# Performance work log

Measured on AMD Instinct MI355X. Metric: run time of the kernel, lower is better.

The kernel has to match this reference:

```python
import jax, jax.numpy as jnp
import numpy as np

N = 100000
E = 1600000
F_IN = 128
F_OUT = 200


def setup_inputs() -> dict:
    key = jax.random.key(0)
    ks = jax.random.split(key, 10)
    x = jax.random.normal(ks[0], (N, F_IN), dtype=jnp.float32)
    edge_index = jax.random.randint(ks[1], (2, E), 0, N, dtype=jnp.int64)
    edge_weight = jax.random.uniform(ks[2], (E,), dtype=jnp.float32)
    s = 1.0 / np.sqrt(F_IN)
    W1 = jax.random.uniform(ks[3], (1, F_IN, F_OUT), dtype=jnp.float32, minval=-s, maxval=s)
    b1 = jnp.zeros((F_OUT,), dtype=jnp.float32)
    W2 = jax.random.uniform(ks[4], (2, F_IN, F_OUT), dtype=jnp.float32, minval=-s, maxval=s)
    b2 = jnp.zeros((F_OUT,), dtype=jnp.float32)
    W3 = jax.random.uniform(ks[5], (3, F_IN, F_OUT), dtype=jnp.float32, minval=-s, maxval=s)
    b3 = jnp.zeros((F_OUT,), dtype=jnp.float32)
    return {"x": x, "edge_index": edge_index, "edge_weight": edge_weight,
            "W1": W1, "b1": b1, "W2": W2, "b2": b2, "W3": W3, "b3": b3}


def _cheb_norm(edge_index, edge_weight, n):
    # PyG ChebConv norm with lambda_max=2.0: scaled Laplacian L_hat = L - I
    # off-diagonal entries: -w_ij * d_i^{-1/2} * d_j^{-1/2}; diagonal: 0
    row, col = edge_index[0], edge_index[1]
    deg = jax.ops.segment_sum(edge_weight, row, num_segments=n)
    dis = jnp.where(deg > 0, jax.lax.rsqrt(jnp.where(deg > 0, deg, 1.0)), 0.0)
    return -edge_weight * dis[row] * dis[col]


def _propagate(h, row, col, norm, n):
    # h: [N, F] -> sum over incoming edges of norm_e * h[col_e]
    return jax.ops.segment_sum(norm[:, None] * h[col], row, num_segments=n)


def _chebconv(x, row, col, norm, W, b, n):
    K = W.shape[0]
    Tx_prev2 = x
    out = jnp.einsum('nf,fo->no', x, W[0])
    if K > 1:
        Tx_prev = _propagate(x, row, col, norm, n)
        out = out + jnp.einsum('nf,fo->no', Tx_prev, W[1])
        for k in range(2, K):
            Tx_k = 2.0 * _propagate(Tx_prev, row, col, norm, n) - Tx_prev2
            out = out + jnp.einsum('nf,fo->no', Tx_k, W[k])
            Tx_prev2, Tx_prev = Tx_prev, Tx_k
    return out + b


def reference(x, edge_index, edge_weight, W1, b1, W2, b2, W3, b3):
    n = x.shape[0]
    row, col = edge_index[0], edge_index[1]
    norm = _cheb_norm(edge_index, edge_weight, n)
    scale_1 = _chebconv(x, row, col, norm, W1, b1, n)
    scale_2 = _chebconv(x, row, col, norm, W2, b2, n)
    scale_3 = _chebconv(x, row, col, norm, W3, b3, n)
    return (scale_1, scale_2, scale_3)
```

## Files before the change

kernel.cpp:

```cpp
#include <hip/hip_runtime.h>
#include <hip/hip_bf16.h>
#include <stdint.h>

#define NN    100000
#define NROWP 100096
#define NE    1600000
#define FIN   128
#define FOUT  200
#define NBLK  391

typedef __attribute__((ext_vector_type(8))) short short8;
typedef __attribute__((ext_vector_type(8))) unsigned short ushort8;
typedef __attribute__((ext_vector_type(2))) float f32x2;
typedef __attribute__((ext_vector_type(4))) float f32x4;
typedef __attribute__((ext_vector_type(2))) unsigned int u32x2;
typedef __attribute__((ext_vector_type(4))) unsigned int uint32x4;

__device__ __forceinline__ short f2bf(float f) {
    __hip_bfloat16 h = __float2bfloat16(f);
    return *reinterpret_cast<short*>(&h);
}
__device__ __forceinline__ unsigned short f2bfu(float f) {
    __hip_bfloat16 h = __float2bfloat16(f);
    return *reinterpret_cast<unsigned short*>(&h);
}
__device__ __forceinline__ float bf2f(unsigned short u) {
    return __uint_as_float((unsigned)u << 16);
}
__device__ __forceinline__ int getidx(const void* ei, int isI32, long long i) {
    return isI32 ? ((const int*)ei)[i] : (int)((const long long*)ei)[i];
}

__global__ void detect_kernel(const long long* ei64, int* flag) {
    int t = blockIdx.x * blockDim.x + threadIdx.x;
    long long v = ei64[t];
    if (v < 0 || v >= NN) atomicOr(flag, 1);
}

__global__ void cnt8_kernel(const void* ei, const int* flag, int* cnt8) {
    int e = blockIdx.x * blockDim.x + threadIdx.x;
    int r = getidx(ei, *flag, e);
    atomicAdd(&cnt8[(blockIdx.x & 7) * NN + r], 1);
}

__global__ void xreduce(int* __restrict__ cnt8, int* __restrict__ cnt) {
    int r = blockIdx.x * 256 + threadIdx.x;
    if (r >= NN) return;
    int s = 0;
    #pragma unroll
    for (int x = 0; x < 8; ++x) {
        int v = cnt8[x * NN + r];
        cnt8[x * NN + r] = s;
        s += v;
    }
    cnt[r] = s;
}

__global__ void scan_block(const int* __restrict__ cnt, int* __restrict__ rowstart,
                           int* __restrict__ bsum) {
    __shared__ int tmp[256];
    int i = blockIdx.x * 256 + threadIdx.x;
    int v = (i < NN) ? cnt[i] : 0;
    tmp[threadIdx.x] = v;
    __syncthreads();
    for (int off = 1; off < 256; off <<= 1) {
        int t = (threadIdx.x >= off) ? tmp[threadIdx.x - off] : 0;
        __syncthreads();
        tmp[threadIdx.x] += t;
        __syncthreads();
    }
    if (i < NN) rowstart[i] = tmp[threadIdx.x] - v;
    if (threadIdx.x == 255) bsum[blockIdx.x] = tmp[255];
}

__global__ void scan_bsums(int* bsum) {
    __shared__ int tmp[512];
    int t = threadIdx.x;
    int v = (t < NBLK) ? bsum[t] : 0;
    tmp[t] = v;
    __syncthreads();
    for (int off = 1; off < 512; off <<= 1) {
        int u = (t >= off) ? tmp[t - off] : 0;
        __syncthreads();
        tmp[t] += u;
        __syncthreads();
    }
    if (t < NBLK) bsum[t] = tmp[t] - v;
}

__global__ void scan_add(int* __restrict__ rowstart, const int* __restrict__ bsum) {
    int i = blockIdx.x * 256 + threadIdx.x;
    if (i < NN)       rowstart[i] += bsum[i >> 8];
    else if (i == NN) rowstart[NN] = NE;
}

__global__ void fill_csr(const void* ei, const int* flag, const float* __restrict__ w,
                         const int* __restrict__ rowstart, int* __restrict__ cnt8,
                         int2* __restrict__ edge) {
    int e = blockIdx.x * blockDim.x + threadIdx.x;
    int isI32 = *flag;
    int r = getidx(ei, isI32, e);
    int c = getidx(ei, isI32, (long long)NE + e);
    int pos = rowstart[r] + atomicAdd(&cnt8[(blockIdx.x & 7) * NN + r], 1);
    int2 rec; rec.x = c; rec.y = __float_as_int(w[e]);
    edge[pos] = rec;
}

__global__ void deg_seg(const int* __restrict__ rowstart, const int2* __restrict__ edge,
                        float* __restrict__ dis) {
    int r = blockIdx.x * 256 + threadIdx.x;
    if (r >= NN) return;
    int s = rowstart[r], e = rowstart[r + 1];
    float d = 0.f;
    for (int i = s; i < e; ++i) d += __int_as_float(edge[i].y);
    dis[r] = d > 0.f ? rsqrtf(d) : 0.f;
}

__global__ void xconv_kernel(const float* __restrict__ x, const float* __restrict__ dis,
                             unsigned short* __restrict__ xb, unsigned int* __restrict__ xs8) {
    int i = blockIdx.x * 256 + threadIdx.x;
    float d = dis[i >> 4];
    long long base = (long long)i * 8;
    f32x4 v0 = *(const f32x4*)(x + base);
    f32x4 v1 = *(const f32x4*)(x + base + 4);
    ushort8 o;
    #pragma unroll
    for (int k = 0; k < 4; ++k) { o[k] = f2bfu(v0[k]); o[4 + k] = f2bfu(v1[k]); }
    __builtin_nontemporal_store(o, (ushort8*)(xb + base));
    unsigned u0 = __builtin_amdgcn_cvt_pk_fp8_f32(d * v0[0], d * v0[1], 0, false);
    u0 = __builtin_amdgcn_cvt_pk_fp8_f32(d * v0[2], d * v0[3], u0, true);
    unsigned u1 = __builtin_amdgcn_cvt_pk_fp8_f32(d * v1[0], d * v1[1], 0, false);
    u1 = __builtin_amdgcn_cvt_pk_fp8_f32(d * v1[2], d * v1[3], u1, true);
    u32x2 ov; ov[0] = u0; ov[1] = u1;
    __builtin_nontemporal_store(ov, (u32x2*)(xs8 + (long long)i * 2));
}

template <int MODE>
__launch_bounds__(256)
__global__ void gather_prop(const int* __restrict__ rowstart, const int2* __restrict__ edge,
                            const float* __restrict__ dis,
                            const unsigned int* __restrict__ src8,
                            const unsigned short* __restrict__ xb,
                            unsigned short* __restrict__ dstb,
                            unsigned int* __restrict__ dst8) {
    int gw   = (blockIdx.x << 2) + (threadIdx.x >> 6);
    int lane = threadIdx.x & 63;
    int q = lane >> 4, fl = lane & 15;
    int s = rowstart[gw], eend = rowstart[gw + 1];
    float a0[8] = {0.f,0.f,0.f,0.f,0.f,0.f,0.f,0.f};
    float a1[8] = {0.f,0.f,0.f,0.f,0.f,0.f,0.f,0.f};
    int e = s + q;
    for (; e + 4 < eend; e += 8) {
        int2 ed0 = edge[e];
        int2 ed1 = edge[e + 4];
        u32x2 v0 = *(const u32x2*)(src8 + ((long long)ed0.x << 5) + (fl << 1));
        u32x2 v1 = *(const u32x2*)(src8 + ((long long)ed1.x << 5) + (fl << 1));
        float w0 = __int_as_float(ed0.y);
        float w1 = __int_as_float(ed1.y);
        f32x2 p0 = __builtin_amdgcn_cvt_pk_f32_fp8(v0[0], false);
        f32x2 p1 = __builtin_amdgcn_cvt_pk_f32_fp8(v0[0], true);
        f32x2 p2 = __builtin_amdgcn_cvt_pk_f32_fp8(v0[1], false);
        f32x2 p3 = __builtin_amdgcn_cvt_pk_f32_fp8(v0[1], true);
        a0[0] += w0 * p0.x; a0[1] += w0 * p0.y; a0[2] += w0 * p1.x; a0[3] += w0 * p1.y;
        a0[4] += w0 * p2.x; a0[5] += w0 * p2.y; a0[6] += w0 * p3.x; a0[7] += w0 * p3.y;
        f32x2 r0 = __builtin_amdgcn_cvt_pk_f32_fp8(v1[0], false);
        f32x2 r1 = __builtin_amdgcn_cvt_pk_f32_fp8(v1[0], true);
        f32x2 r2 = __builtin_amdgcn_cvt_pk_f32_fp8(v1[1], false);
        f32x2 r3 = __builtin_amdgcn_cvt_pk_f32_fp8(v1[1], true);
        a1[0] += w1 * r0.x; a1[1] += w1 * r0.y; a1[2] += w1 * r1.x; a1[3] += w1 * r1.y;
        a1[4] += w1 * r2.x; a1[5] += w1 * r2.y; a1[6] += w1 * r3.x; a1[7] += w1 * r3.y;
    }
    if (e < eend) {
        int2 ed = edge[e];
        u32x2 v = *(const u32x2*)(src8 + ((long long)ed.x << 5) + (fl << 1));
        float w = __int_as_float(ed.y);
        f32x2 p0 = __builtin_amdgcn_cvt_pk_f32_fp8(v[0], false);
        f32x2 p1 = __builtin_amdgcn_cvt_pk_f32_fp8(v[0], true);
        f32x2 p2 = __builtin_amdgcn_cvt_pk_f32_fp8(v[1], false);
        f32x2 p3 = __builtin_amdgcn_cvt_pk_f32_fp8(v[1], true);
        a0[0] += w * p0.x; a0[1] += w * p0.y; a0[2] += w * p1.x; a0[3] += w * p1.y;
        a0[4] += w * p2.x; a0[5] += w * p2.y; a0[6] += w * p3.x; a0[7] += w * p3.y;
    }
    #pragma unroll
    for (int i = 0; i < 8; ++i) {
        a0[i] += a1[i];
        a0[i] += __shfl_xor(a0[i], 16);
        a0[i] += __shfl_xor(a0[i], 32);
    }
    if (lane < 16) {
        float sr = -dis[gw];
        if (MODE == 1) {
            ushort8 xv = *(const ushort8*)(xb + ((long long)gw << 7) + (fl << 3));
            ushort8 o;
            #pragma unroll
            for (int i = 0; i < 8; ++i) o[i] = f2bfu(2.f * sr * a0[i] - bf2f(xv[i]));
            __builtin_nontemporal_store(o, (ushort8*)(dstb + ((long long)gw << 7) + (fl << 3)));
        } else {
            float t[8];
            ushort8 o;
            #pragma unroll
            for (int i = 0; i < 8; ++i) { t[i] = sr * a0[i]; o[i] = f2bfu(t[i]); }
            __builtin_nontemporal_store(o, (ushort8*)(dstb + ((long long)gw << 7) + (fl << 3)));
            float ds = dis[gw];
            unsigned u0 = __builtin_amdgcn_cvt_pk_fp8_f32(ds * t[0], ds * t[1], 0, false);
            u0 = __builtin_amdgcn_cvt_pk_fp8_f32(ds * t[2], ds * t[3], u0, true);
            unsigned u1 = __builtin_amdgcn_cvt_pk_fp8_f32(ds * t[4], ds * t[5], 0, false);
            u1 = __builtin_amdgcn_cvt_pk_fp8_f32(ds * t[6], ds * t[7], u1, true);
            u32x2 ov; ov[0] = u0; ov[1] = u1;
            __builtin_nontemporal_store(ov, (u32x2*)(dst8 + ((long long)gw << 5) + (fl << 1)));
        }
    }
}

__global__ void wprep_frag(const float* __restrict__ W1, const float* __restrict__ W2,
                           const float* __restrict__ W3, short* __restrict__ Wf) {
    __shared__ float lds[32 * 200];
    int bid = blockIdx.x;
    int s, ks;
    if (bid < 4)       { s = 0; ks = bid; }
    else if (bid < 12) { s = 1; ks = bid - 4; }
    else               { s = 2; ks = bid - 12; }
    const float* W = (s == 0) ? W1 : ((s == 1) ? W2 : W3);
    int p = ks >> 2;
    const float* Wp = W + (p * 128 + (ks & 3) * 32) * 200;
    for (int e = threadIdx.x; e < 6400; e += 256) lds[e] = Wp[e];
    __syncthreads();
    int nk = (s + 1) * 4;
    int fb = (s == 0) ? 0 : ((s == 1) ? 52 : 156);
    for (int qq = threadIdx.x; qq < 13 * 64; qq += 256) {
        int t = qq >> 6, lane = qq & 63;
        int col = t * 16 + (lane & 15);
        int kb  = (lane >> 4) * 8;
        short8 v;
        #pragma unroll
        for (int i = 0; i < 8; ++i) {
            float f = (col < FOUT) ? lds[(kb + i) * 200 + col] : 0.f;
            v[i] = f2bf(f);
        }
        *(short8*)&Wf[(fb + t * nk + ks) * 512 + lane * 8] = v;
    }
}

__constant__ int u_sc[8][5] = {
    {2,2,1,0,0}, {2,2,1,0,0}, {2,2,1,0,0}, {2,2,1,0,0},
    {2,2,1,0,0}, {2,2,1,0,0}, {2,1,1,1,0}, {1,1,1,1,-1}};
__constant__ int u_t[8][5] = {
    {0,1,0,0,1},     {2,3,1,2,3},    {4,5,2,4,5},    {6,7,3,6,7},
    {8,9,4,8,9},     {10,11,5,10,11},{12,6,7,8,12},  {9,10,11,12,0}};

#define EPAD 212

__launch_bounds__(512, 2)
__global__ void gemm_fused(const unsigned short* __restrict__ xb,
                           const unsigned short* __restrict__ t1b,
                           const unsigned short* __restrict__ t2b,
                           const short* __restrict__ Wf,
                           const float* __restrict__ b1, const float* __restrict__ b2,
                           const float* __restrict__ b3, float* __restrict__ out) {
    __shared__ __align__(16) char smem[64 * EPAD * 4];
    short* As = (short*)smem;
    float* Ef = (float*)smem;

    const int tid  = threadIdx.x;
    const int wave = tid >> 6;
    const int lane = tid & 63;
    const int l15  = lane & 15;
    const int lhi  = lane >> 4;
    const int b0   = blockIdx.x * 64;

    const unsigned short* panels[3] = {xb, t1b, t2b};
    #pragma unroll
    for (int i = 0; i < 6; ++i) {
        int q   = i * 512 + tid;
        int p   = q >> 10;
        int rem = q & 1023;
        int row = rem >> 4;
        int ch  = rem & 15;
        uint32x4 v = *(const uint32x4*)(panels[p] + ((long long)(b0 + row) << 7) + (ch << 3));
        *(uint32x4*)&As[((p * 64 + row) * 16 + (ch ^ (row & 7))) * 8] = v;
    }

    int usc[5], ubase[5], ucol0[5];
    #pragma unroll
    for (int j = 0; j < 5; ++j) {
        int sc = u_sc[wave][j], t = u_t[wave][j];
        usc[j]   = sc;
        ucol0[j] = t * 16;
        int nk = 4 * (sc + 1);
        int fb = (sc == 0) ? 0 : ((sc == 1) ? 52 : 156);
        ubase[j] = fb + t * nk;
    }

    f32x4 acc[5][4];
    #pragma unroll
    for (int j = 0; j < 5; ++j)
        #pragma unroll
        for (int m = 0; m < 4; ++m) acc[j][m] = {0.f, 0.f, 0.f, 0.f};

    short8 bf[2][5];
    #pragma unroll
    for (int j = 0; j < 5; ++j)
        bf[0][j] = *(const short8*)(Wf + (long long)(ubase[j] + 0) * 512 + lane * 8);

    __syncthreads();

    #pragma unroll
    for (int step = 0; step < 12; ++step) {
        const int p   = step >> 2;
        const int k4  = step & 3;
        const int cur = step & 1;
        if (step < 11) {
            #pragma unroll
            for (int j = 0; j < 5; ++j)
                bf[cur ^ 1][j] = *(const short8*)(Wf + (long long)(ubase[j] + step + 1) * 512 + lane * 8);
        }
        short8 af[4];
        #pragma unroll
        for (int m = 0; m < 4; ++m) {
            int row = m * 16 + l15;
            int ch  = (k4 * 4 + lhi) ^ (row & 7);
            af[m] = *(const short8*)&As[((p * 64 + row) * 16 + ch) * 8];
        }
        #pragma unroll
        for (int j = 0; j < 5; ++j) {
            if (usc[j] >= p) {
                #pragma unroll
                for (int m = 0; m < 4; ++m)
                    acc[j][m] = __builtin_amdgcn_mfma_f32_16x16x32_bf16(af[m], bf[cur][j], acc[j][m], 0, 0, 0);
            }
        }
    }

    #pragma unroll 1
    for (int sc = 0; sc < 3; ++sc) {
        __syncthreads();
        const float* bias = (sc == 0) ? b1 : ((sc == 1) ? b2 : b3);
        #pragma unroll
        for (int j = 0; j < 5; ++j) {
            if (usc[j] == sc) {
                int col = ucol0[j] + l15;
                if (col < FOUT) {
                    float bv = bias[col];
                    #pragma unroll
                    for (int m = 0; m < 4; ++m) {
                        int rbase = m * 16 + lhi * 4;
                        #pragma unroll
                        for (int jj = 0; jj < 4; ++jj)
                            Ef[(rbase + jj) * EPAD + col] = acc[j][m][jj] + bv;
                    }
                }
            }
        }
        __syncthreads();
        float* op = out + (long long)sc * NN * FOUT;
        for (int c = tid; c < 3200; c += 512) {
            int r = c / 50, pos = c % 50;
            int row = b0 + r;
            if (row < NN) {
                f32x4 v = *(const f32x4*)&Ef[r * EPAD + pos * 4];
                __builtin_nontemporal_store(v, (f32x4*)&op[(long long)row * FOUT + pos * 4]);
            }
        }
    }
}

extern "C" void kernel_launch(void* const* d_in, const int* in_sizes, int n_in,
                              void* d_out, int out_size, void* d_ws, size_t ws_size,
                              hipStream_t stream) {
    const float* x  = (const float*)d_in[0];
    const void*  ei = d_in[1];
    const float* ew = (const float*)d_in[2];
    const float* W1 = (const float*)d_in[3];
    const float* b1 = (const float*)d_in[4];
    const float* W2 = (const float*)d_in[5];
    const float* b2 = (const float*)d_in[6];
    const float* W3 = (const float*)d_in[7];
    const float* b3 = (const float*)d_in[8];
    float* out = (float*)d_out;

    char* ws = (char*)d_ws;
    int*   flag     = (int*)(ws + 0);
    int*   cnt8     = (int*)(ws + 16);
    int*   cnt      = (int*)(ws + 3200016);
    int*   rowstart = (int*)(ws + 3600016);
    int*   bsum     = (int*)(ws + 4000032);
    float* dis      = (float*)(ws + 4002080);
    int2*  edge     = (int2*)(ws + 4402080);
    unsigned short* Xb  = (unsigned short*)(ws + 17202080);
    unsigned short* T1b = (unsigned short*)(ws + 42826656);
    unsigned short* T2b = (unsigned short*)(ws + 68451232);
    short* Wf       = (short*)(ws + 94075808);
    unsigned int* Xs8  = (unsigned int*)(ws + 94395296);
    unsigned int* T1s8 = (unsigned int*)(ws + 107207584);

    hipMemsetAsync(d_ws, 0, 3200016, stream);

    detect_kernel<<<16, 256, 0, stream>>>((const long long*)ei, flag);
    cnt8_kernel<<<NE / 256, 256, 0, stream>>>(ei, flag, cnt8);
    xreduce<<<NBLK, 256, 0, stream>>>(cnt8, cnt);
    scan_block<<<NBLK, 256, 0, stream>>>(cnt, rowstart, bsum);
    scan_bsums<<<1, 512, 0, stream>>>(bsum);
    scan_add<<<NBLK + 1, 256, 0, stream>>>(rowstart, bsum);
    fill_csr<<<NE / 256, 256, 0, stream>>>(ei, flag, ew, rowstart, cnt8, edge);
    deg_seg<<<NBLK, 256, 0, stream>>>(rowstart, edge, dis);
    xconv_kernel<<<6250, 256, 0, stream>>>(x, dis, Xb, Xs8);
    gather_prop<0><<<NN / 4, 256, 0, stream>>>(rowstart, edge, dis, Xs8, nullptr, T1b, T1s8);
    gather_prop<1><<<NN / 4, 256, 0, stream>>>(rowstart, edge, dis, T1s8, Xb, T2b, nullptr);
    wprep_frag<<<24, 256, 0, stream>>>(W1, W2, W3, Wf);
    gemm_fused<<<1563, 512, 0, stream>>>(Xb, T1b, T2b, Wf, b1, b2, b3, out);
}
```

Baseline: 420.1 us.

## Widen gather loads to 16 bytes, fuse count reduction into scan, tweak LDS pad

The gather kernel now has each lane load 16 fp8 features (128-bit) per edge, with 8 edge slots per wave instead of 4. This halves the feature lanes per row and adds one extra shuffle stage to the reduction. The per-row count reduction kernel is folded into the block scan kernel, which removes one launch and one intermediate array. The GEMM epilogue LDS padding is also changed from 212 to 204, which may alter bank conflicts.

```diff
diff --git a/kernel.cpp b/kernel.cpp
--- a/kernel.cpp
+++ b/kernel.cpp
@@ -43,24 +43,21 @@
     atomicAdd(&cnt8[(blockIdx.x & 7) * NN + r], 1);
 }
 
-__global__ void xreduce(int* __restrict__ cnt8, int* __restrict__ cnt) {
-    int r = blockIdx.x * 256 + threadIdx.x;
-    if (r >= NN) return;
-    int s = 0;
-    #pragma unroll
-    for (int x = 0; x < 8; ++x) {
-        int v = cnt8[x * NN + r];
-        cnt8[x * NN + r] = s;
-        s += v;
-    }
-    cnt[r] = s;
-}
-
-__global__ void scan_block(const int* __restrict__ cnt, int* __restrict__ rowstart,
+__global__ void scan_block(int* __restrict__ cnt8, int* __restrict__ rowstart,
                            int* __restrict__ bsum) {
     __shared__ int tmp[256];
     int i = blockIdx.x * 256 + threadIdx.x;
-    int v = (i < NN) ? cnt[i] : 0;
+    int v = 0;
+    if (i < NN) {
+        int s = 0;
+        #pragma unroll
+        for (int x = 0; x < 8; ++x) {
+            int c = cnt8[x * NN + i];
+            cnt8[x * NN + i] = s;
+            s += c;
+        }
+        v = s;
+    }
     tmp[threadIdx.x] = v;
     __syncthreads();
     for (int off = 1; off < 256; off <<= 1) {
@@ -145,69 +142,85 @@
                             unsigned int* __restrict__ dst8) {
     int gw   = (blockIdx.x << 2) + (threadIdx.x >> 6);
     int lane = threadIdx.x & 63;
-    int q = lane >> 4, fl = lane & 15;
+    int slot = lane >> 3, fl = lane & 7;
     int s = rowstart[gw], eend = rowstart[gw + 1];
-    float a0[8] = {0.f,0.f,0.f,0.f,0.f,0.f,0.f,0.f};
-    float a1[8] = {0.f,0.f,0.f,0.f,0.f,0.f,0.f,0.f};
-    int e = s + q;
-    for (; e + 4 < eend; e += 8) {
+    float a0[16], a1[16];
+    #pragma unroll
+    for (int i = 0; i < 16; ++i) { a0[i] = 0.f; a1[i] = 0.f; }
+    int e = s + slot;
+    for (; e + 8 < eend; e += 16) {
         int2 ed0 = edge[e];
-        int2 ed1 = edge[e + 4];
-        u32x2 v0 = *(const u32x2*)(src8 + ((long long)ed0.x << 5) + (fl << 1));
-        u32x2 v1 = *(const u32x2*)(src8 + ((long long)ed1.x << 5) + (fl << 1));
+        int2 ed1 = edge[e + 8];
+        uint32x4 v0 = *(const uint32x4*)(src8 + ((long long)ed0.x << 5) + (fl << 2));
+        uint32x4 v1 = *(const uint32x4*)(src8 + ((long long)ed1.x << 5) + (fl << 2));
         float w0 = __int_as_float(ed0.y);
         float w1 = __int_as_float(ed1.y);
-        f32x2 p0 = __builtin_amdgcn_cvt_pk_f32_fp8(v0[0], false);
-        f32x2 p1 = __builtin_amdgcn_cvt_pk_f32_fp8(v0[0], true);
-        f32x2 p2 = __builtin_amdgcn_cvt_pk_f32_fp8(v0[1], false);
-        f32x2 p3 = __builtin_amdgcn_cvt_pk_f32_fp8(v0[1], true);
-        a0[0] += w0 * p0.x; a0[1] += w0 * p0.y; a0[2] += w0 * p1.x; a0[3] += w0 * p1.y;
-        a0[4] += w0 * p2.x; a0[5] += w0 * p2.y; a0[6] += w0 * p3.x; a0[7] += w0 * p3.y;
-        f32x2 r0 = __builtin_amdgcn_cvt_pk_f32_fp8(v1[0], false);
-        f32x2 r1 = __builtin_amdgcn_cvt_pk_f32_fp8(v1[0], true);
-        f32x2 r2 = __builtin_amdgcn_cvt_pk_f32_fp8(v1[1], false);
-        f32x2 r3 = __builtin_amdgcn_cvt_pk_f32_fp8(v1[1], true);
-        a1[0] += w1 * r0.x; a1[1] += w1 * r0.y; a1[2] += w1 * r1.x; a1[3] += w1 * r1.y;
-        a1[4] += w1 * r2.x; a1[5] += w1 * r2.y; a1[6] += w1 * r3.x; a1[7] += w1 * r3.y;
+        #pragma unroll
+        for (int u = 0; u < 4; ++u) {
+            f32x2 lo0 = __builtin_amdgcn_cvt_pk_f32_fp8(v0[u], false);
+            f32x2 hi0 = __builtin_amdgcn_cvt_pk_f32_fp8(v0[u], true);
+            a0[u*4+0] += w0 * lo0.x; a0[u*4+1] += w0 * lo0.y;
+            a0[u*4+2] += w0 * hi0.x; a0[u*4+3] += w0 * hi0.y;
+            f32x2 lo1 = __builtin_amdgcn_cvt_pk_f32_fp8(v1[u], false);
+            f32x2 hi1 = __builtin_amdgcn_cvt_pk_f32_fp8(v1[u], true);
+            a1[u*4+0] += w1 * lo1.x; a1[u*4+1] += w1 * lo1.y;
+            a1[u*4+2] += w1 * hi1.x; a1[u*4+3] += w1 * hi1.y;
+        }
     }
     if (e < eend) {
         int2 ed = edge[e];
-        u32x2 v = *(const u32x2*)(src8 + ((long long)ed.x << 5) + (fl << 1));
+        uint32x4 v = *(const uint32x4*)(src8 + ((long long)ed.x << 5) + (fl << 2));
         float w = __int_as_float(ed.y);
-        f32x2 p0 = __builtin_amdgcn_cvt_pk_f32_fp8(v[0], false);
-        f32x2 p1 = __builtin_amdgcn_cvt_pk_f32_fp8(v[0], true);
-        f32x2 p2 = __builtin_amdgcn_cvt_pk_f32_fp8(v[1], false);
-        f32x2 p3 = __builtin_amdgcn_cvt_pk_f32_fp8(v[1], true);
-        a0[0] += w * p0.x; a0[1] += w * p0.y; a0[2] += w * p1.x; a0[3] += w * p1.y;
-        a0[4] += w * p2.x; a0[5] += w * p2.y; a0[6] += w * p3.x; a0[7] += w * p3.y;
-    }
-    #pragma unroll
-    for (int i = 0; i < 8; ++i) {
+        #pragma unroll
+        for (int u = 0; u < 4; ++u) {
+            f32x2 lo = __builtin_amdgcn_cvt_pk_f32_fp8(v[u], false);
+            f32x2 hi = __builtin_amdgcn_cvt_pk_f32_fp8(v[u], true);
+            a0[u*4+0] += w * lo.x; a0[u*4+1] += w * lo.y;
+            a0[u*4+2] += w * hi.x; a0[u*4+3] += w * hi.y;
+        }
+    }
+    #pragma unroll
+    for (int i = 0; i < 16; ++i) {
         a0[i] += a1[i];
+        a0[i] += __shfl_xor(a0[i], 8);
         a0[i] += __shfl_xor(a0[i], 16);
         a0[i] += __shfl_xor(a0[i], 32);
     }
-    if (lane < 16) {
+    if (lane < 8) {
         float sr = -dis[gw];
+        long long rb = ((long long)gw << 7) + (fl << 4);
         if (MODE == 1) {
-            ushort8 xv = *(const ushort8*)(xb + ((long long)gw << 7) + (fl << 3));
-            ushort8 o;
+            ushort8 xv0 = *(const ushort8*)(xb + rb);
+            ushort8 xv1 = *(const ushort8*)(xb + rb + 8);
+            ushort8 o0, o1;
             #pragma unroll
-            for (int i = 0; i < 8; ++i) o[i] = f2bfu(2.f * sr * a0[i] - bf2f(xv[i]));
-            __builtin_nontemporal_store(o, (ushort8*)(dstb + ((long long)gw << 7) + (fl << 3)));
+            for (int i = 0; i < 8; ++i) {
+                o0[i] = f2bfu(2.f * sr * a0[i]     - bf2f(xv0[i]));
+                o1[i] = f2bfu(2.f * sr * a0[8 + i] - bf2f(xv1[i]));
+            }
+            __builtin_nontemporal_store(o0, (ushort8*)(dstb + rb));
+            __builtin_nontemporal_store(o1, (ushort8*)(dstb + rb + 8));
         } else {
-            float t[8];
-            ushort8 o;
+            float t[16];
+            ushort8 o0, o1;
             #pragma unroll
-            for (int i = 0; i < 8; ++i) { t[i] = sr * a0[i]; o[i] = f2bfu(t[i]); }
-            __builtin_nontemporal_store(o, (ushort8*)(dstb + ((long long)gw << 7) + (fl << 3)));
+            for (int i = 0; i < 8; ++i) {
+                t[i] = sr * a0[i]; t[8 + i] = sr * a0[8 + i];
+                o0[i] = f2bfu(t[i]); o1[i] = f2bfu(t[8 + i]);
+            }
+            __builtin_nontemporal_store(o0, (ushort8*)(dstb + rb));
+            __builtin_nontemporal_store(o1, (ushort8*)(dstb + rb + 8));
             float ds = dis[gw];
-            unsigned u0 = __builtin_amdgcn_cvt_pk_fp8_f32(ds * t[0], ds * t[1], 0, false);
-            u0 = __builtin_amdgcn_cvt_pk_fp8_f32(ds * t[2], ds * t[3], u0, true);
-            unsigned u1 = __builtin_amdgcn_cvt_pk_fp8_f32(ds * t[4], ds * t[5], 0, false);
-            u1 = __builtin_amdgcn_cvt_pk_fp8_f32(ds * t[6], ds * t[7], u1, true);
-            u32x2 ov; ov[0] = u0; ov[1] = u1;
-            __builtin_nontemporal_store(ov, (u32x2*)(dst8 + ((long long)gw << 5) + (fl << 1)));
+            unsigned q0 = __builtin_amdgcn_cvt_pk_fp8_f32(ds * t[0],  ds * t[1],  0, false);
+            q0 = __builtin_amdgcn_cvt_pk_fp8_f32(ds * t[2],  ds * t[3],  q0, true);
+            unsigned q1 = __builtin_amdgcn_cvt_pk_fp8_f32(ds * t[4],  ds * t[5],  0, false);
+            q1 = __builtin_amdgcn_cvt_pk_fp8_f32(ds * t[6],  ds * t[7],  q1, true);
+            unsigned q2 = __builtin_amdgcn_cvt_pk_fp8_f32(ds * t[8],  ds * t[9],  0, false);
+            q2 = __builtin_amdgcn_cvt_pk_fp8_f32(ds * t[10], ds * t[11], q2, true);
+            unsigned q3 = __builtin_amdgcn_cvt_pk_fp8_f32(ds * t[12], ds * t[13], 0, false);
+            q3 = __builtin_amdgcn_cvt_pk_fp8_f32(ds * t[14], ds * t[15], q3, true);
+            uint32x4 ov; ov[0] = q0; ov[1] = q1; ov[2] = q2; ov[3] = q3;
+            __builtin_nontemporal_store(ov, (uint32x4*)(dst8 + ((long long)gw << 5) + (fl << 2)));
         }
     }
 }
@@ -248,7 +261,7 @@
     {0,1,0,0,1},     {2,3,1,2,3},    {4,5,2,4,5},    {6,7,3,6,7},
     {8,9,4,8,9},     {10,11,5,10,11},{12,6,7,8,12},  {9,10,11,12,0}};
 
-#define EPAD 212
+#define EPAD 204
 
 __launch_bounds__(512, 2)
 __global__ void gemm_fused(const unsigned short* __restrict__ xb,
@@ -381,7 +394,6 @@
     char* ws = (char*)d_ws;
     int*   flag     = (int*)(ws + 0);
     int*   cnt8     = (int*)(ws + 16);
-    int*   cnt      = (int*)(ws + 3200016);
     int*   rowstart = (int*)(ws + 3600016);
     int*   bsum     = (int*)(ws + 4000032);
     float* dis      = (float*)(ws + 4002080);
@@ -397,8 +409,7 @@
 
     detect_kernel<<<16, 256, 0, stream>>>((const long long*)ei, flag);
     cnt8_kernel<<<NE / 256, 256, 0, stream>>>(ei, flag, cnt8);
-    xreduce<<<NBLK, 256, 0, stream>>>(cnt8, cnt);
-    scan_block<<<NBLK, 256, 0, stream>>>(cnt, rowstart, bsum);
+    scan_block<<<NBLK, 256, 0, stream>>>(cnt8, rowstart, bsum);
     scan_bsums<<<1, 512, 0, stream>>>(bsum);
     scan_add<<<NBLK + 1, 256, 0, stream>>>(rowstart, bsum);
     fill_csr<<<NE / 256, 256, 0, stream>>>(ei, flag, ew, rowstart, cnt8, edge);
```

Result: slower. 445.3 us (+6.0%).
